# Kernel tuning notes

Hardware: AMD Instinct MI355X
Metric: run time of the kernel (lower is better)

The kernel has to match this reference:

```python
import jax, jax.numpy as jnp
import numpy as np

N_NODES = 100000
N_EDGES = 1600000
N_PAIRS = 500000
D_IN = 64
D_HID = 64
N_CLASSES = 2


def setup_inputs() -> dict:
    key = jax.random.key(0)
    ks = jax.random.split(key, 16)
    s = 1.0 / np.sqrt(D_HID)
    inp = {
        "h": jax.random.normal(ks[0], (N_NODES, D_IN), dtype=jnp.float32),
        "src": jax.random.randint(ks[1], (N_EDGES,), 0, N_NODES, dtype=jnp.int32),
        "dst": jax.random.randint(ks[2], (N_EDGES,), 0, N_NODES, dtype=jnp.int32),
        "x1": jax.random.randint(ks[3], (N_PAIRS,), 0, N_NODES, dtype=jnp.int32),
        "x2": jax.random.randint(ks[4], (N_PAIRS,), 0, N_NODES, dtype=jnp.int32),
        # SAGEConv layer 0: fc_self + fc_neigh + bias
        "W_self0": jax.random.normal(ks[5], (D_IN, D_HID), dtype=jnp.float32) * s,
        "W_neigh0": jax.random.normal(ks[6], (D_IN, D_HID), dtype=jnp.float32) * s,
        "b0": jnp.zeros((D_HID,), dtype=jnp.float32),
        # SAGEConv layer 1
        "W_self1": jax.random.normal(ks[7], (D_HID, D_HID), dtype=jnp.float32) * s,
        "W_neigh1": jax.random.normal(ks[8], (D_HID, D_HID), dtype=jnp.float32) * s,
        "b1": jnp.zeros((D_HID,), dtype=jnp.float32),
        # MLP head: linear1 (3*D_HID -> D_HID), linear2 (D_HID -> N_CLASSES)
        "W1": jax.random.normal(ks[9], (3 * D_HID, D_HID), dtype=jnp.float32) * (1.0 / np.sqrt(3 * D_HID)),
        "b_l1": jnp.zeros((D_HID,), dtype=jnp.float32),
        "W2": jax.random.normal(ks[10], (D_HID, N_CLASSES), dtype=jnp.float32) * s,
        "b_l2": jnp.zeros((N_CLASSES,), dtype=jnp.float32),
    }
    return inp


def reference(h, src, dst, x1, x2, W_self0, W_neigh0, b0, W_self1, W_neigh1, b1, W1, b_l1, W2, b_l2):
    N = h.shape[0]
    # in-degree per destination node (clamped to avoid div-by-zero; DGL mean agg)
    deg = jax.ops.segment_sum(jnp.ones((src.shape[0],), h.dtype), dst, num_segments=N)
    deg = jnp.maximum(deg, 1.0)[:, None]  # [N, 1]

    def sage(feat, Ws, Wn, b):
        # mean aggregation of neighbor features over edges src -> dst
        neigh = jax.ops.segment_sum(feat[src], dst, num_segments=N) / deg  # [N, d]
        return jax.nn.relu(feat @ Ws + neigh @ Wn + b)

    h = sage(h, W_self0, W_neigh0, b0)
    h = sage(h, W_self1, W_neigh1, b1)

    h1, h2 = h[x1], h[x2]  # [P, d]
    e = jnp.concatenate([h1, h2, jnp.abs(h1 - h2)], axis=1)  # [P, 3d]
    out = jax.nn.relu(e @ W1 + b_l1) @ W2 + b_l2  # [P, n_classes]
    return out
```

## Files before the change

### kernel.cpp

```cpp
#include <hip/hip_runtime.h>
#include <hip/hip_bf16.h>

using s8v = __attribute__((ext_vector_type(8))) short;
using f4v = __attribute__((ext_vector_type(4))) float;

__device__ __forceinline__ float bf2f(ushort v) { return __uint_as_float(((unsigned)v) << 16); }
__device__ __forceinline__ ushort f2bf(float x) {
  unsigned u = __float_as_uint(x);
  return (ushort)((u + 0x7fffu + ((u >> 16) & 1u)) >> 16);
}

#define BSH 9
#define NPB 512
#define MAXB 256
#define CHUNK 4096


__global__ __launch_bounds__(256) void k_prep(
    const float* __restrict__ h, const float* __restrict__ W1,
    const float* __restrict__ Ws0, const float* __restrict__ Wn0,
    const float* __restrict__ Ws1, const float* __restrict__ Wn1,
    ushort* __restrict__ h_bf, ushort* __restrict__ w1t,
    ushort* __restrict__ tS0, ushort* __restrict__ tN0,
    ushort* __restrict__ tS1, ushort* __restrict__ tN1,
    int* __restrict__ bucketCnt, int n8)
{
  int i = blockIdx.x * 256 + threadIdx.x;
  if (i < MAXB) bucketCnt[i] = 0;
  if (i < 4096) {
    int j = i >> 6, k = i & 63;
    int o = k * 64 + j;
    tS0[i] = f2bf(Ws0[o]);
    tN0[i] = f2bf(Wn0[o]);
    tS1[i] = f2bf(Ws1[o]);
    tN1[i] = f2bf(Wn1[o]);
  }
  if (i < 64 * 200) {
    int n = i / 200, k = i % 200;
    float v = (k < 192) ? W1[k * 64 + n] : 0.f;
    w1t[i] = f2bf(v);
  }
  if (i < n8) {
    const float4* in4 = (const float4*)h;
    float4 va = in4[2 * i], vb = in4[2 * i + 1];
    s8v w;
    w[0] = (short)f2bf(va.x); w[1] = (short)f2bf(va.y);
    w[2] = (short)f2bf(va.z); w[3] = (short)f2bf(va.w);
    w[4] = (short)f2bf(vb.x); w[5] = (short)f2bf(vb.y);
    w[6] = (short)f2bf(vb.z); w[7] = (short)f2bf(vb.w);
    ((s8v*)h_bf)[i] = w;
  }
}


__global__ __launch_bounds__(256) void k_hist(const int* __restrict__ dst,
                                              int* __restrict__ bucketCnt, int E) {
  __shared__ int hh[MAXB];
  int t = threadIdx.x;
  hh[t] = 0;
  __syncthreads();
  int base = blockIdx.x * CHUNK;
  #pragma unroll
  for (int k = 0; k < CHUNK / 256; ++k) {
    int e = base + k * 256 + t;
    if (e < E) atomicAdd(&hh[dst[e] >> BSH], 1);
  }
  __syncthreads();
  int c = hh[t];
  if (c) atomicAdd(&bucketCnt[t], c);
}


__global__ __launch_bounds__(256) void k_bscan(const int* __restrict__ bucketCnt,
                                               int* __restrict__ bucketBase,
                                               int* __restrict__ bucketCursor,
                                               int* __restrict__ row_ptr,
                                               int B, int N, int E) {
  __shared__ int sh[MAXB];
  int t = threadIdx.x;
  int v = (t < B) ? bucketCnt[t] : 0;
  sh[t] = v;
  __syncthreads();
  for (int off = 1; off < MAXB; off <<= 1) {
    int y = (t >= off) ? sh[t - off] : 0;
    __syncthreads();
    sh[t] += y;
    __syncthreads();
  }
  int excl = sh[t] - v;
  if (t < B) { bucketBase[t] = excl; bucketCursor[t] = excl; }
  if (t == 0) { bucketBase[B] = E; row_ptr[N] = E; }
}


__global__ __launch_bounds__(256) void k_part(
    const int* __restrict__ src, const int* __restrict__ dst,
    int* __restrict__ bucketCursor, int2* __restrict__ stag, int E)
{
  __shared__ int hh[MAXB];
  __shared__ int sc[MAXB];
  __shared__ int cur[MAXB];
  __shared__ int gb[MAXB];
  __shared__ int2 pairs[CHUNK];

  int t = threadIdx.x;
  int base = blockIdx.x * CHUNK;
  int M = E - base; if (M > CHUNK) M = CHUNK;

  int es[CHUNK / 256], ed[CHUNK / 256];
  #pragma unroll
  for (int k = 0; k < CHUNK / 256; ++k) {
    int e = base + k * 256 + t;
    if (e < E) { es[k] = src[e]; ed[k] = dst[e]; } else { ed[k] = -1; }
  }

  hh[t] = 0;
  __syncthreads();
  #pragma unroll
  for (int k = 0; k < CHUNK / 256; ++k)
    if (ed[k] >= 0) atomicAdd(&hh[ed[k] >> BSH], 1);
  __syncthreads();

  int v = hh[t];
  sc[t] = v;
  __syncthreads();
  for (int off = 1; off < MAXB; off <<= 1) {
    int y = (t >= off) ? sc[t - off] : 0;
    __syncthreads();
    sc[t] += y;
    __syncthreads();
  }
  int excl = sc[t] - v;
  sc[t] = excl;
  cur[t] = excl;
  if (v) gb[t] = atomicAdd(&bucketCursor[t], v);
  __syncthreads();

  #pragma unroll
  for (int k = 0; k < CHUNK / 256; ++k)
    if (ed[k] >= 0) {
      int b = ed[k] >> BSH;
      int pos = atomicAdd(&cur[b], 1);
      pairs[pos] = make_int2(es[k], ed[k]);
    }
  __syncthreads();

  for (int s = t; s < M; s += 256) {
    int2 pr = pairs[s];
    int b = pr.y >> BSH;
    stag[gb[b] + s - sc[b]] = pr;
  }
}


__global__ __launch_bounds__(512) void k_csr_bucket(
    const int2* __restrict__ stag, const int* __restrict__ bucketBase,
    int* __restrict__ row_ptr, int* __restrict__ csr_src, int N)
{
  __shared__ int dh[NPB], db[NPB], dc[NPB];
  int t = threadIdx.x;
  int b = blockIdx.x;
  int n0 = b << BSH;
  int nn = N - n0; if (nn > NPB) nn = NPB;
  int estart = bucketBase[b], eend = bucketBase[b + 1];

  dh[t] = 0;
  __syncthreads();
  for (int e = estart + t; e < eend; e += 512)
    atomicAdd(&dh[stag[e].y - n0], 1);
  __syncthreads();
  int v = dh[t];
  db[t] = v;
  __syncthreads();
  for (int off = 1; off < NPB; off <<= 1) {
    int y = (t >= off) ? db[t - off] : 0;
    __syncthreads();
    db[t] += y;
    __syncthreads();
  }
  int excl = db[t] - v;
  if (t < nn) row_ptr[n0 + t] = estart + excl;
  dc[t] = excl;
  __syncthreads();
  for (int e = estart + t; e < eend; e += 512) {
    int2 pr = stag[e];
    int d = pr.y - n0;
    int pos = estart + atomicAdd(&dc[d], 1);
    csr_src[pos] = pr.x;
  }
}


__global__ __launch_bounds__(256) void k_agg_bf(
    const ushort* __restrict__ fb, const int* __restrict__ rp,
    const int* __restrict__ csrc, ushort* __restrict__ agg, int N)
{
  int lane = threadIdx.x & 63;
  int node = (blockIdx.x * 256 + threadIdx.x) >> 6;
  if (node >= N) return;
  int g  = lane >> 3;
  int c8 = (lane & 7) * 8;
  int e0 = rp[node], e1 = rp[node + 1];
  int len = e1 - e0;
  float a0=0.f,a1=0.f,a2=0.f,a3=0.f,a4=0.f,a5=0.f,a6=0.f,a7=0.f;
  int nfull = len >> 3;
  int it = 0;
  int e = e0;
  for (; it + 2 <= nfull; it += 2, e += 16) {
    int sA = csrc[e + g];
    int sB = csrc[e + 8 + g];
    s8v va = *(const s8v*)(fb + (size_t)sA * 64 + c8);
    s8v vb = *(const s8v*)(fb + (size_t)sB * 64 + c8);
    a0 += bf2f((ushort)va[0]); a1 += bf2f((ushort)va[1]);
    a2 += bf2f((ushort)va[2]); a3 += bf2f((ushort)va[3]);
    a4 += bf2f((ushort)va[4]); a5 += bf2f((ushort)va[5]);
    a6 += bf2f((ushort)va[6]); a7 += bf2f((ushort)va[7]);
    a0 += bf2f((ushort)vb[0]); a1 += bf2f((ushort)vb[1]);
    a2 += bf2f((ushort)vb[2]); a3 += bf2f((ushort)vb[3]);
    a4 += bf2f((ushort)vb[4]); a5 += bf2f((ushort)vb[5]);
    a6 += bf2f((ushort)vb[6]); a7 += bf2f((ushort)vb[7]);
  }
  if (it < nfull) {
    int s = csrc[e + g];
    s8v vv = *(const s8v*)(fb + (size_t)s * 64 + c8);
    a0 += bf2f((ushort)vv[0]); a1 += bf2f((ushort)vv[1]);
    a2 += bf2f((ushort)vv[2]); a3 += bf2f((ushort)vv[3]);
    a4 += bf2f((ushort)vv[4]); a5 += bf2f((ushort)vv[5]);
    a6 += bf2f((ushort)vv[6]); a7 += bf2f((ushort)vv[7]);
    e += 8;
  }
  if (e + g < e1) {
    int s = csrc[e + g];
    s8v vv = *(const s8v*)(fb + (size_t)s * 64 + c8);
    a0 += bf2f((ushort)vv[0]); a1 += bf2f((ushort)vv[1]);
    a2 += bf2f((ushort)vv[2]); a3 += bf2f((ushort)vv[3]);
    a4 += bf2f((ushort)vv[4]); a5 += bf2f((ushort)vv[5]);
    a6 += bf2f((ushort)vv[6]); a7 += bf2f((ushort)vv[7]);
  }
  a0 += __shfl_xor(a0, 8); a0 += __shfl_xor(a0, 16); a0 += __shfl_xor(a0, 32);
  a1 += __shfl_xor(a1, 8); a1 += __shfl_xor(a1, 16); a1 += __shfl_xor(a1, 32);
  a2 += __shfl_xor(a2, 8); a2 += __shfl_xor(a2, 16); a2 += __shfl_xor(a2, 32);
  a3 += __shfl_xor(a3, 8); a3 += __shfl_xor(a3, 16); a3 += __shfl_xor(a3, 32);
  a4 += __shfl_xor(a4, 8); a4 += __shfl_xor(a4, 16); a4 += __shfl_xor(a4, 32);
  a5 += __shfl_xor(a5, 8); a5 += __shfl_xor(a5, 16); a5 += __shfl_xor(a5, 32);
  a6 += __shfl_xor(a6, 8); a6 += __shfl_xor(a6, 16); a6 += __shfl_xor(a6, 32);
  a7 += __shfl_xor(a7, 8); a7 += __shfl_xor(a7, 16); a7 += __shfl_xor(a7, 32);
  if (g == 0) {
    float inv = 1.f / (float)(len > 0 ? len : 1);
    s8v o;
    o[0] = (short)f2bf(a0 * inv); o[1] = (short)f2bf(a1 * inv);
    o[2] = (short)f2bf(a2 * inv); o[3] = (short)f2bf(a3 * inv);
    o[4] = (short)f2bf(a4 * inv); o[5] = (short)f2bf(a5 * inv);
    o[6] = (short)f2bf(a6 * inv); o[7] = (short)f2bf(a7 * inv);
    *(s8v*)(agg + (size_t)node * 64 + c8) = o;
  }
}


__global__ __launch_bounds__(256) void k_xform_mfma(
    const ushort* __restrict__ fb, const ushort* __restrict__ ab,
    const ushort* __restrict__ wtS, const ushort* __restrict__ wtN,
    const float* __restrict__ bias, ushort* __restrict__ outb, int N)
{
  int lane = threadIdx.x & 63;
  int wid  = threadIdx.x >> 6;
  int wbase = blockIdx.x * 128 + wid * 32;
  if (wbase >= N) return;
  int lrow = lane & 15;
  int lkg  = lane >> 4;

  s8v bS[4][2], bN[4][2];
  #pragma unroll
  for (int nt = 0; nt < 4; ++nt) {
    #pragma unroll
    for (int ks = 0; ks < 2; ++ks) {
      int o = (nt * 16 + lrow) * 64 + ks * 32 + lkg * 8;
      bS[nt][ks] = *(const s8v*)(wtS + o);
      bN[nt][ks] = *(const s8v*)(wtN + o);
    }
  }

  f4v acc[2][4];
  #pragma unroll
  for (int a = 0; a < 2; ++a)
    #pragma unroll
    for (int b = 0; b < 4; ++b)
      acc[a][b] = (f4v){0.f, 0.f, 0.f, 0.f};

  #pragma unroll
  for (int pt = 0; pt < 2; ++pt) {
    int node = wbase + pt * 16 + lrow;
    int nc = (node < N) ? node : (N - 1);
    const ushort* fr = fb + (size_t)nc * 64 + lkg * 8;
    const ushort* ar = ab + (size_t)nc * 64 + lkg * 8;
    s8v f0 = *(const s8v*)(fr);
    s8v f1 = *(const s8v*)(fr + 32);
    s8v g0 = *(const s8v*)(ar);
    s8v g1 = *(const s8v*)(ar + 32);
    #pragma unroll
    for (int nt = 0; nt < 4; ++nt) {
      acc[pt][nt] = __builtin_amdgcn_mfma_f32_16x16x32_bf16(f0, bS[nt][0], acc[pt][nt], 0, 0, 0);
      acc[pt][nt] = __builtin_amdgcn_mfma_f32_16x16x32_bf16(f1, bS[nt][1], acc[pt][nt], 0, 0, 0);
      acc[pt][nt] = __builtin_amdgcn_mfma_f32_16x16x32_bf16(g0, bN[nt][0], acc[pt][nt], 0, 0, 0);
      acc[pt][nt] = __builtin_amdgcn_mfma_f32_16x16x32_bf16(g1, bN[nt][1], acc[pt][nt], 0, 0, 0);
    }
  }

  float bv[4];
  #pragma unroll
  for (int nt = 0; nt < 4; ++nt) bv[nt] = bias[nt * 16 + lrow];

  #pragma unroll
  for (int pt = 0; pt < 2; ++pt) {
    #pragma unroll
    for (int r = 0; r < 4; ++r) {
      int node = wbase + pt * 16 + lkg * 4 + r;
      if (node < N) {
        ushort* orow = outb + (size_t)node * 64;
        #pragma unroll
        for (int nt = 0; nt < 4; ++nt) {
          float z = fmaxf(acc[pt][nt][r] + bv[nt], 0.f);
          orow[nt * 16 + lrow] = f2bf(z);
        }
      }
    }
  }
}


__global__ __launch_bounds__(256) void k_head_mfma(
    const ushort* __restrict__ hb, const int* __restrict__ x1, const int* __restrict__ x2,
    const ushort* __restrict__ w1t, const float* __restrict__ bl1,
    const float* __restrict__ W2, const float* __restrict__ bl2,
    float* __restrict__ out, int P)
{
  __shared__ __align__(16) ushort sW[64 * 200];
  __shared__ float sW2[128];
  __shared__ float sb1[64];
  __shared__ float sb2[2];
  {
    const float4* srcv = (const float4*)w1t;
    float4* dstv = (float4*)sW;
    for (int i = threadIdx.x; i < 1600; i += 256) dstv[i] = srcv[i];
    if (threadIdx.x < 128) sW2[threadIdx.x] = W2[threadIdx.x];
    if (threadIdx.x < 64)  sb1[threadIdx.x] = bl1[threadIdx.x];
    if (threadIdx.x < 2)   sb2[threadIdx.x] = bl2[threadIdx.x];
  }
  __syncthreads();

  int lane = threadIdx.x & 63;
  int wid  = threadIdx.x >> 6;
  int wbase = blockIdx.x * 128 + wid * 32;
  if (wbase >= P) return;

  int lrow = lane & 15;
  int lkg  = lane >> 4;

  f4v acc[2][4];
  #pragma unroll
  for (int a = 0; a < 2; ++a)
    #pragma unroll
    for (int b = 0; b < 4; ++b)
      acc[a][b] = (f4v){0.f, 0.f, 0.f, 0.f};

  #pragma unroll
  for (int pt = 0; pt < 2; ++pt) {
    int p = wbase + pt * 16 + lrow;
    int pc = (p < P) ? p : (P - 1);
    int i1 = x1[pc], i2 = x2[pc];
    const ushort* r1 = hb + (size_t)i1 * 64 + lkg * 8;
    const ushort* r2 = hb + (size_t)i2 * 64 + lkg * 8;
    s8v a1_0 = *(const s8v*)(r1);
    s8v a1_1 = *(const s8v*)(r1 + 32);
    s8v a2_0 = *(const s8v*)(r2);
    s8v a2_1 = *(const s8v*)(r2 + 32);
    s8v d0, d1;
    #pragma unroll
    for (int j = 0; j < 8; ++j) {
      d0[j] = (short)f2bf(fabsf(bf2f((ushort)a1_0[j]) - bf2f((ushort)a2_0[j])));
      d1[j] = (short)f2bf(fabsf(bf2f((ushort)a1_1[j]) - bf2f((ushort)a2_1[j])));
    }
    #pragma unroll
    for (int nt = 0; nt < 4; ++nt) {
      const ushort* bw = &sW[(nt * 16 + lrow) * 200 + lkg * 8];
      s8v b1_0 = *(const s8v*)(bw + 0);
      s8v b2_0 = *(const s8v*)(bw + 64);
      s8v b3_0 = *(const s8v*)(bw + 128);
      acc[pt][nt] = __builtin_amdgcn_mfma_f32_16x16x32_bf16(a1_0, b1_0, acc[pt][nt], 0, 0, 0);
      acc[pt][nt] = __builtin_amdgcn_mfma_f32_16x16x32_bf16(a2_0, b2_0, acc[pt][nt], 0, 0, 0);
      acc[pt][nt] = __builtin_amdgcn_mfma_f32_16x16x32_bf16(d0,   b3_0, acc[pt][nt], 0, 0, 0);
      s8v b1_1 = *(const s8v*)(bw + 32);
      s8v b2_1 = *(const s8v*)(bw + 96);
      s8v b3_1 = *(const s8v*)(bw + 160);
      acc[pt][nt] = __builtin_amdgcn_mfma_f32_16x16x32_bf16(a1_1, b1_1, acc[pt][nt], 0, 0, 0);
      acc[pt][nt] = __builtin_amdgcn_mfma_f32_16x16x32_bf16(a2_1, b2_1, acc[pt][nt], 0, 0, 0);
      acc[pt][nt] = __builtin_amdgcn_mfma_f32_16x16x32_bf16(d1,   b3_1, acc[pt][nt], 0, 0, 0);
    }
  }

  float b1v[4], w20v[4], w21v[4];
  #pragma unroll
  for (int nt = 0; nt < 4; ++nt) {
    int n = nt * 16 + lrow;
    b1v[nt] = sb1[n];
    w20v[nt] = sW2[2 * n + 0];
    w21v[nt] = sW2[2 * n + 1];
  }
  float bb0 = sb2[0], bb1 = sb2[1];
  #pragma unroll
  for (int pt = 0; pt < 2; ++pt) {
    #pragma unroll
    for (int r = 0; r < 4; ++r) {
      float p0 = 0.f, p1 = 0.f;
      #pragma unroll
      for (int nt = 0; nt < 4; ++nt) {
        float z = fmaxf(acc[pt][nt][r] + b1v[nt], 0.f);
        p0 += z * w20v[nt];
        p1 += z * w21v[nt];
      }
      p0 += __shfl_xor(p0, 1); p1 += __shfl_xor(p1, 1);
      p0 += __shfl_xor(p0, 2); p1 += __shfl_xor(p1, 2);
      p0 += __shfl_xor(p0, 4); p1 += __shfl_xor(p1, 4);
      p0 += __shfl_xor(p0, 8); p1 += __shfl_xor(p1, 8);
      int pair = wbase + pt * 16 + lkg * 4 + r;
      if (lrow == 0 && pair < P) {
        float2 o = make_float2(p0 + bb0, p1 + bb1);
        *(float2*)(out + 2 * (size_t)pair) = o;
      }
    }
  }
}


extern "C" void kernel_launch(void* const* d_in, const int* in_sizes, int n_in,
                              void* d_out, int out_size, void* d_ws, size_t ws_size,
                              hipStream_t stream)
{
  (void)n_in; (void)out_size; (void)ws_size;
  const float* h   = (const float*)d_in[0];
  const int*   src = (const int*)d_in[1];
  const int*   dst = (const int*)d_in[2];
  const int*   x1  = (const int*)d_in[3];
  const int*   x2  = (const int*)d_in[4];
  const float* Ws0 = (const float*)d_in[5];
  const float* Wn0 = (const float*)d_in[6];
  const float* b0  = (const float*)d_in[7];
  const float* Ws1 = (const float*)d_in[8];
  const float* Wn1 = (const float*)d_in[9];
  const float* b1  = (const float*)d_in[10];
  const float* W1  = (const float*)d_in[11];
  const float* bl1 = (const float*)d_in[12];
  const float* W2  = (const float*)d_in[13];
  const float* bl2 = (const float*)d_in[14];

  const int N = in_sizes[0] / 64;
  const int E = in_sizes[1];
  const int P = in_sizes[3];
  const int B = (N + NPB - 1) >> BSH;
  float* out = (float*)d_out;

  char* ws = (char*)d_ws;
  size_t off = 0;
  auto carve = [&](size_t bytes) {
    char* p = ws + off;
    off = (off + bytes + 255) & ~(size_t)255;
    return p;
  };
  int*    row_ptr      = (int*)carve((size_t)(N + 1) * 4);
  int*    bucketCnt    = (int*)carve(MAXB * 4);
  int*    bucketBase   = (int*)carve((MAXB + 1) * 4);
  int*    bucketCursor = (int*)carve(MAXB * 4);
  int*    csr_src  = (int*)carve((size_t)E * 4);
  ushort* h_bf     = (ushort*)carve((size_t)N * 64 * 2);
  ushort* m1       = (ushort*)carve((size_t)N * 64 * 2);
  ushort* m2       = (ushort*)carve((size_t)N * 64 * 2);
  int2*   stag     = (int2*)carve((size_t)E * 8);
  ushort* aggb     = (ushort*)carve((size_t)N * 64 * 2);
  ushort* w1t      = (ushort*)carve(64 * 200 * 2);
  ushort* wtS0     = (ushort*)carve(4096 * 2);
  ushort* wtN0     = (ushort*)carve(4096 * 2);
  ushort* wtS1     = (ushort*)carve(4096 * 2);
  ushort* wtN1     = (ushort*)carve(4096 * 2);

  const int NCH = (E + CHUNK - 1) / CHUNK;
  const int n8  = N * 64 / 8;

  k_prep<<<(n8 + 255) / 256, 256, 0, stream>>>(h, W1, Ws0, Wn0, Ws1, Wn1,
                                               h_bf, w1t, wtS0, wtN0, wtS1, wtN1,
                                               bucketCnt, n8);
  k_hist <<<NCH, 256, 0, stream>>>(dst, bucketCnt, E);
  k_bscan<<<1, MAXB, 0, stream>>>(bucketCnt, bucketBase, bucketCursor, row_ptr, B, N, E);
  k_part <<<NCH, 256, 0, stream>>>(src, dst, bucketCursor, stag, E);
  k_csr_bucket<<<B, NPB, 0, stream>>>(stag, bucketBase, row_ptr, csr_src, N);

  const int nbW = (N + 3) / 4;
  const int nbX = (N + 127) / 128;

  k_agg_bf<<<nbW, 256, 0, stream>>>(h_bf, row_ptr, csr_src, aggb, N);
  k_xform_mfma<<<nbX, 256, 0, stream>>>(h_bf, aggb, wtS0, wtN0, b0, m1, N);
  k_agg_bf<<<nbW, 256, 0, stream>>>(m1, row_ptr, csr_src, aggb, N);
  k_xform_mfma<<<nbX, 256, 0, stream>>>(m1, aggb, wtS1, wtN1, b1, m2, N);

  const int nbP = (P + 127) / 128;
  k_head_mfma<<<nbP, 256, 0, stream>>>(m2, x1, x2, w1t, bl1, W2, bl2, out, P);
}
```

Baseline: 205.3 us.

## Fuse histogram into prep kernel and stream head weights from global memory

```diff
diff --git a/kernel.cpp b/kernel.cpp
--- a/kernel.cpp
+++ b/kernel.cpp
@@ -10,6 +10,20 @@
   return (ushort)((u + 0x7fffu + ((u >> 16) & 1u)) >> 16);
 }
 
+__device__ __forceinline__ s8v absdiff_bf(s8v x, s8v y) {
+  s8v d;
+  #pragma unroll
+  for (int q = 0; q < 4; ++q) {
+    float f0 = fabsf(bf2f((ushort)x[2*q+0]) - bf2f((ushort)y[2*q+0]));
+    float f1 = fabsf(bf2f((ushort)x[2*q+1]) - bf2f((ushort)y[2*q+1]));
+    unsigned w;
+    asm("v_cvt_pk_bf16_f32 %0, %1, %2" : "=v"(w) : "v"(f0), "v"(f1));
+    d[2*q+0] = (short)(w & 0xffffu);
+    d[2*q+1] = (short)(w >> 16);
+  }
+  return d;
+}
+
 #define BSH 9
 #define NPB 512
 #define MAXB 256
@@ -20,13 +34,16 @@
     const float* __restrict__ h, const float* __restrict__ W1,
     const float* __restrict__ Ws0, const float* __restrict__ Wn0,
     const float* __restrict__ Ws1, const float* __restrict__ Wn1,
+    const int* __restrict__ dst,
     ushort* __restrict__ h_bf, ushort* __restrict__ w1t,
     ushort* __restrict__ tS0, ushort* __restrict__ tN0,
     ushort* __restrict__ tS1, ushort* __restrict__ tN1,
-    int* __restrict__ bucketCnt, int n8)
-{
-  int i = blockIdx.x * 256 + threadIdx.x;
-  if (i < MAXB) bucketCnt[i] = 0;
+    int* __restrict__ bucketCnt, int n8, int E, int nch)
+{
+  __shared__ int hh[MAXB];
+  int t = threadIdx.x;
+  int i = blockIdx.x * 256 + t;
+
   if (i < 4096) {
     int j = i >> 6, k = i & 63;
     int o = k * 64 + j;
@@ -35,10 +52,9 @@
     tS1[i] = f2bf(Ws1[o]);
     tN1[i] = f2bf(Wn1[o]);
   }
-  if (i < 64 * 200) {
-    int n = i / 200, k = i % 200;
-    float v = (k < 192) ? W1[k * 64 + n] : 0.f;
-    w1t[i] = f2bf(v);
+  if (i < 64 * 192) {
+    int n = i / 192, k = i % 192;
+    w1t[i] = f2bf(W1[k * 64 + n]);
   }
   if (i < n8) {
     const float4* in4 = (const float4*)h;
@@ -50,24 +66,19 @@
     w[6] = (short)f2bf(vb.z); w[7] = (short)f2bf(vb.w);
     ((s8v*)h_bf)[i] = w;
   }
-}
-
-
-__global__ __launch_bounds__(256) void k_hist(const int* __restrict__ dst,
-                                              int* __restrict__ bucketCnt, int E) {
-  __shared__ int hh[MAXB];
-  int t = threadIdx.x;
-  hh[t] = 0;
-  __syncthreads();
-  int base = blockIdx.x * CHUNK;
-  #pragma unroll
-  for (int k = 0; k < CHUNK / 256; ++k) {
-    int e = base + k * 256 + t;
-    if (e < E) atomicAdd(&hh[dst[e] >> BSH], 1);
-  }
-  __syncthreads();
-  int c = hh[t];
-  if (c) atomicAdd(&bucketCnt[t], c);
+  if (blockIdx.x < (unsigned)nch) {
+    hh[t] = 0;
+    __syncthreads();
+    int base = blockIdx.x * CHUNK;
+    #pragma unroll
+    for (int k = 0; k < CHUNK / 256; ++k) {
+      int e = base + k * 256 + t;
+      if (e < E) atomicAdd(&hh[dst[e] >> BSH], 1);
+    }
+    __syncthreads();
+    int c = hh[t];
+    if (c) atomicAdd(&bucketCnt[t], c);
+  }
 }
 
 
@@ -334,20 +345,6 @@
     const float* __restrict__ W2, const float* __restrict__ bl2,
     float* __restrict__ out, int P)
 {
-  __shared__ __align__(16) ushort sW[64 * 200];
-  __shared__ float sW2[128];
-  __shared__ float sb1[64];
-  __shared__ float sb2[2];
-  {
-    const float4* srcv = (const float4*)w1t;
-    float4* dstv = (float4*)sW;
-    for (int i = threadIdx.x; i < 1600; i += 256) dstv[i] = srcv[i];
-    if (threadIdx.x < 128) sW2[threadIdx.x] = W2[threadIdx.x];
-    if (threadIdx.x < 64)  sb1[threadIdx.x] = bl1[threadIdx.x];
-    if (threadIdx.x < 2)   sb2[threadIdx.x] = bl2[threadIdx.x];
-  }
-  __syncthreads();
-
   int lane = threadIdx.x & 63;
   int wid  = threadIdx.x >> 6;
   int wbase = blockIdx.x * 128 + wid * 32;
@@ -356,6 +353,30 @@
   int lrow = lane & 15;
   int lkg  = lane >> 4;
 
+  int pa = wbase + lrow;
+  int pb = wbase + 16 + lrow;
+  int pca = (pa < P) ? pa : (P - 1);
+  int pcb = (pb < P) ? pb : (P - 1);
+  int i1a = x1[pca], i2a = x2[pca];
+  int i1b = x1[pcb], i2b = x2[pcb];
+  const ushort* r1a = hb + (size_t)i1a * 64 + lkg * 8;
+  const ushort* r2a = hb + (size_t)i2a * 64 + lkg * 8;
+  const ushort* r1b = hb + (size_t)i1b * 64 + lkg * 8;
+  const ushort* r2b = hb + (size_t)i2b * 64 + lkg * 8;
+  s8v a1a0 = *(const s8v*)(r1a);
+  s8v a1a1 = *(const s8v*)(r1a + 32);
+  s8v a2a0 = *(const s8v*)(r2a);
+  s8v a2a1 = *(const s8v*)(r2a + 32);
+  s8v a1b0 = *(const s8v*)(r1b);
+  s8v a1b1 = *(const s8v*)(r1b + 32);
+  s8v a2b0 = *(const s8v*)(r2b);
+  s8v a2b1 = *(const s8v*)(r2b + 32);
+
+  s8v da0 = absdiff_bf(a1a0, a2a0);
+  s8v da1 = absdiff_bf(a1a1, a2a1);
+  s8v db0 = absdiff_bf(a1b0, a2b0);
+  s8v db1 = absdiff_bf(a1b1, a2b1);
+
   f4v acc[2][4];
   #pragma unroll
   for (int a = 0; a < 2; ++a)
@@ -364,37 +385,29 @@
       acc[a][b] = (f4v){0.f, 0.f, 0.f, 0.f};
 
   #pragma unroll
-  for (int pt = 0; pt < 2; ++pt) {
-    int p = wbase + pt * 16 + lrow;
-    int pc = (p < P) ? p : (P - 1);
-    int i1 = x1[pc], i2 = x2[pc];
-    const ushort* r1 = hb + (size_t)i1 * 64 + lkg * 8;
-    const ushort* r2 = hb + (size_t)i2 * 64 + lkg * 8;
-    s8v a1_0 = *(const s8v*)(r1);
-    s8v a1_1 = *(const s8v*)(r1 + 32);
-    s8v a2_0 = *(const s8v*)(r2);
-    s8v a2_1 = *(const s8v*)(r2 + 32);
-    s8v d0, d1;
-    #pragma unroll
-    for (int j = 0; j < 8; ++j) {
-      d0[j] = (short)f2bf(fabsf(bf2f((ushort)a1_0[j]) - bf2f((ushort)a2_0[j])));
-      d1[j] = (short)f2bf(fabsf(bf2f((ushort)a1_1[j]) - bf2f((ushort)a2_1[j])));
-    }
-    #pragma unroll
-    for (int nt = 0; nt < 4; ++nt) {
-      const ushort* bw = &sW[(nt * 16 + lrow) * 200 + lkg * 8];
+  for (int nh = 0; nh < 2; ++nh) {
+    #pragma unroll
+    for (int j = 0; j < 2; ++j) {
+      int nt = nh * 2 + j;
+      const ushort* bw = w1t + (size_t)(nt * 16 + lrow) * 192 + lkg * 8;
       s8v b1_0 = *(const s8v*)(bw + 0);
+      s8v b1_1 = *(const s8v*)(bw + 32);
       s8v b2_0 = *(const s8v*)(bw + 64);
+      s8v b2_1 = *(const s8v*)(bw + 96);
       s8v b3_0 = *(const s8v*)(bw + 128);
-      acc[pt][nt] = __builtin_amdgcn_mfma_f32_16x16x32_bf16(a1_0, b1_0, acc[pt][nt], 0, 0, 0);
-      acc[pt][nt] = __builtin_amdgcn_mfma_f32_16x16x32_bf16(a2_0, b2_0, acc[pt][nt], 0, 0, 0);
-      acc[pt][nt] = __builtin_amdgcn_mfma_f32_16x16x32_bf16(d0,   b3_0, acc[pt][nt], 0, 0, 0);
-      s8v b1_1 = *(const s8v*)(bw + 32);
-      s8v b2_1 = *(const s8v*)(bw + 96);
       s8v b3_1 = *(const s8v*)(bw + 160);
-      acc[pt][nt] = __builtin_amdgcn_mfma_f32_16x16x32_bf16(a1_1, b1_1, acc[pt][nt], 0, 0, 0);
-      acc[pt][nt] = __builtin_amdgcn_mfma_f32_16x16x32_bf16(a2_1, b2_1, acc[pt][nt], 0, 0, 0);
-      acc[pt][nt] = __builtin_amdgcn_mfma_f32_16x16x32_bf16(d1,   b3_1, acc[pt][nt], 0, 0, 0);
+      acc[0][nt] = __builtin_amdgcn_mfma_f32_16x16x32_bf16(a1a0, b1_0, acc[0][nt], 0, 0, 0);
+      acc[0][nt] = __builtin_amdgcn_mfma_f32_16x16x32_bf16(a1a1, b1_1, acc[0][nt], 0, 0, 0);
+      acc[0][nt] = __builtin_amdgcn_mfma_f32_16x16x32_bf16(a2a0, b2_0, acc[0][nt], 0, 0, 0);
+      acc[0][nt] = __builtin_amdgcn_mfma_f32_16x16x32_bf16(a2a1, b2_1, acc[0][nt], 0, 0, 0);
+      acc[0][nt] = __builtin_amdgcn_mfma_f32_16x16x32_bf16(da0,  b3_0, acc[0][nt], 0, 0, 0);
+      acc[0][nt] = __builtin_amdgcn_mfma_f32_16x16x32_bf16(da1,  b3_1, acc[0][nt], 0, 0, 0);
+      acc[1][nt] = __builtin_amdgcn_mfma_f32_16x16x32_bf16(a1b0, b1_0, acc[1][nt], 0, 0, 0);
+      acc[1][nt] = __builtin_amdgcn_mfma_f32_16x16x32_bf16(a1b1, b1_1, acc[1][nt], 0, 0, 0);
+      acc[1][nt] = __builtin_amdgcn_mfma_f32_16x16x32_bf16(a2b0, b2_0, acc[1][nt], 0, 0, 0);
+      acc[1][nt] = __builtin_amdgcn_mfma_f32_16x16x32_bf16(a2b1, b2_1, acc[1][nt], 0, 0, 0);
+      acc[1][nt] = __builtin_amdgcn_mfma_f32_16x16x32_bf16(db0,  b3_0, acc[1][nt], 0, 0, 0);
+      acc[1][nt] = __builtin_amdgcn_mfma_f32_16x16x32_bf16(db1,  b3_1, acc[1][nt], 0, 0, 0);
     }
   }
 
@@ -402,11 +415,12 @@
   #pragma unroll
   for (int nt = 0; nt < 4; ++nt) {
     int n = nt * 16 + lrow;
-    b1v[nt] = sb1[n];
-    w20v[nt] = sW2[2 * n + 0];
-    w21v[nt] = sW2[2 * n + 1];
-  }
-  float bb0 = sb2[0], bb1 = sb2[1];
+    b1v[nt] = bl1[n];
+    float2 w2 = *(const float2*)(W2 + 2 * n);
+    w20v[nt] = w2.x;
+    w21v[nt] = w2.y;
+  }
+  float bb0 = bl2[0], bb1 = bl2[1];
   #pragma unroll
   for (int pt = 0; pt < 2; ++pt) {
     #pragma unroll
@@ -476,7 +490,7 @@
   ushort* m2       = (ushort*)carve((size_t)N * 64 * 2);
   int2*   stag     = (int2*)carve((size_t)E * 8);
   ushort* aggb     = (ushort*)carve((size_t)N * 64 * 2);
-  ushort* w1t      = (ushort*)carve(64 * 200 * 2);
+  ushort* w1t      = (ushort*)carve(64 * 192 * 2);
   ushort* wtS0     = (ushort*)carve(4096 * 2);
   ushort* wtN0     = (ushort*)carve(4096 * 2);
   ushort* wtS1     = (ushort*)carve(4096 * 2);
@@ -485,10 +499,10 @@
   const int NCH = (E + CHUNK - 1) / CHUNK;
   const int n8  = N * 64 / 8;
 
-  k_prep<<<(n8 + 255) / 256, 256, 0, stream>>>(h, W1, Ws0, Wn0, Ws1, Wn1,
+  hipMemsetAsync(bucketCnt, 0, MAXB * 4, stream);
+  k_prep<<<(n8 + 255) / 256, 256, 0, stream>>>(h, W1, Ws0, Wn0, Ws1, Wn1, dst,
                                                h_bf, w1t, wtS0, wtN0, wtS1, wtN1,
-                                               bucketCnt, n8);
-  k_hist <<<NCH, 256, 0, stream>>>(dst, bucketCnt, E);
+                                               bucketCnt, n8, E, NCH);
   k_bscan<<<1, MAXB, 0, stream>>>(bucketCnt, bucketBase, bucketCursor, row_ptr, B, N, E);
   k_part <<<NCH, 256, 0, stream>>>(src, dst, bucketCursor, stag, E);
   k_csr_bucket<<<B, NPB, 0, stream>>>(stag, bucketBase, row_ptr, csr_src, N);
```

Measured after the change: 232.6 us. 13.3% more time.
